# Kernel tuning notes

Hardware: AMD Instinct MI355X
Metric: run time of the kernel (lower is better)

The kernel has to match this reference:

```python
import jax, jax.numpy as jnp
import numpy as np

# CustomConvLayer with a 3x3-tap .kof file, global defaults:
#   operation: x * w, input_encode: x, kernel_encode: w
# => out[b,o,h,w] = sum_c sum_k x_pad[b,c,h+dh_k,w+dw_k] * weights[o,c,k]
# Tap offsets: integer stencil (dh,dw) in {0,1,2}^2 (k_elems=9), padding=1, stride=1.

PAD = 1
TAPS = [(dh, dw) for dh in range(3) for dw in range(3)]  # 9 taps


def setup_inputs() -> dict:
    key = jax.random.key(0)
    k1, k2 = jax.random.split(key)
    x = jax.random.normal(k1, (16, 64, 128, 128), dtype=jnp.float32)
    # learned per-tap weights: [out_channels, in_channels, k_elems]
    weights = jax.random.normal(k2, (128, 64, 9), dtype=jnp.float32) * 0.05
    return {"x": x, "weights": weights}


def reference(x, weights):
    B, C, H, Wd = x.shape
    xp = jnp.pad(x, ((0, 0), (0, 0), (PAD, PAD), (PAD, PAD)))
    # gather per-tap shifted views: [B, C, K, H, W]
    gathered = jnp.stack([xp[:, :, dh:dh + H, dw:dw + Wd] for dh, dw in TAPS], axis=2)
    # per-tap op x*w, then combine over in_channels and taps
    out = jnp.einsum('bckhw,ock->bohw', gathered, weights)
    return out
```

## Files before the change

### kernel.cpp

```cpp
#include <hip/hip_runtime.h>
#include <hip/hip_bf16.h>
#include <stdint.h>


typedef __bf16 bf16x8 __attribute__((ext_vector_type(8)));
typedef float  f32x4  __attribute__((ext_vector_type(4)));

#define GLD_TO_LDS16(g, l)                                                        \
  __builtin_amdgcn_global_load_lds((const __attribute__((address_space(1))) void*)(g), \
                                   (__attribute__((address_space(3))) void*)(l), 16, 0, 0)

__global__ __launch_bounds__(256) void xform_xw(const float* __restrict__ x,
                                                const float* __restrict__ wgt,
                                                __bf16* __restrict__ xpad,
                                                __bf16* __restrict__ BtF) {
  __shared__ float tile[64][129];
  const int tid = threadIdx.x;
  const int b = blockIdx.x >> 7;
  const int h = blockIdx.x & 127;

  {
    const int t = blockIdx.x * 256 + tid;
    if (t < 9216) {
      const int s = t >> 9, rem = t & 511, quad = rem >> 7, n = rem & 127;
      bf16x8 o;
#pragma unroll
      for (int r = 0; r < 8; ++r) {
        const int k = s * 32 + quad * 8 + r;
        const int tap = k >> 6, c = k & 63;
        o[r] = (__bf16)wgt[(n * 64 + c) * 9 + tap];
      }
      *(bf16x8*)(BtF + (size_t)t * 8) = o;
    }
  }

  const bf16x8 z8 = {};
  __bf16* prow = xpad + (size_t)(b * 130 + h + 1) * 8320;
  if (tid < 8)        *(bf16x8*)(prow + tid * 8) = z8;
  else if (tid < 16)  *(bf16x8*)(prow + 8256 + (tid - 8) * 8) = z8;
  if (h == 0) {
    bf16x8* r0 = (bf16x8*)(xpad + (size_t)(b * 130) * 8320);
    for (int i = tid; i < 1040; i += 256) r0[i] = z8;
  } else if (h == 127) {
    bf16x8* r129 = (bf16x8*)(xpad + (size_t)(b * 130 + 129) * 8320);
    for (int i = tid; i < 1040; i += 256) r129[i] = z8;
  }

  const float* src = x + (((size_t)b * 64) * 128 + h) * 128;
  for (int i = tid; i < 2048; i += 256) {
    const int c = i >> 5, w4 = i & 31;
    f32x4 v = *(const f32x4*)(src + (size_t)c * 16384 + w4 * 4);
    tile[c][w4 * 4 + 0] = v[0];
    tile[c][w4 * 4 + 1] = v[1];
    tile[c][w4 * 4 + 2] = v[2];
    tile[c][w4 * 4 + 3] = v[3];
  }
  __syncthreads();
  __bf16* dst = xpad + ((size_t)(b * 130 + h + 1) * 130 + 1) * 64;
  for (int i = tid; i < 1024; i += 256) {
    const int w = i >> 3, cg = i & 7;
    bf16x8 o;
#pragma unroll
    for (int r = 0; r < 8; ++r) o[r] = (__bf16)tile[cg * 8 + r][w];
    *(bf16x8*)(dst + (size_t)w * 64 + cg * 8) = o;
  }
}

__global__ __launch_bounds__(256) void conv_mfma(const __bf16* __restrict__ xpad,
                                                 const __bf16* __restrict__ BtF,
                                                 float* __restrict__ out) {
  __shared__ alignas(16) __bf16 Aslab[3328 * 8];
  const int tid  = threadIdx.x;
  const int lane = tid & 63;
  const int wave = tid >> 6;
  const int quad = lane >> 4;
  const int l16  = lane & 15;
  const int rank = (blockIdx.x & 7) * 256 + (blockIdx.x >> 3);
  const int b = rank >> 7;
  const int h = rank & 127;
  const int wm = wave >> 1;
  const int wn = wave & 1;

  const __bf16* slab = xpad + ((size_t)(b * 130 + h) * 130) * 64;
#define STAGE_UNIT(U) do {                                                \
    const int l_   = ((U) << 8) + tid;                                    \
    const int v_   = l_ >> 3;                                             \
    const int vc_  = v_ > 389 ? 389 : v_;                                 \
    const int cqs_ = (l_ & 7) ^ (v_ & 7);                                 \
    GLD_TO_LDS16(slab + vc_ * 64 + cqs_ * 8,                              \
                 (char*)Aslab + ((((U) << 2) + wave) << 10));             \
  } while (0)

#pragma unroll
  for (int u = 0; u < 13; ++u) STAGE_UNIT(u);
  __builtin_amdgcn_sched_barrier(0);

  f32x4 acc[4][4] = {};

#define PHASE(DH)                                                              \
  _Pragma("unroll")                                                            \
  for (int dw = 0; dw < 3; ++dw) {                                             \
    _Pragma("unroll")                                                          \
    for (int half = 0; half < 2; ++half) {                                     \
      const int s_  = ((DH) * 3 + dw) * 2 + half;                              \
      const int cq_ = (half << 2) + quad;                                      \
      bf16x8 aF[4], bF[4];          \
      _Pragma("unroll")                                                        \
      for (int i = 0; i < 4; ++i) {                                            \
        const int m_    = (wm << 6) + (i << 4) + l16;                          \
        const int v_    = (DH) * 130 + m_ + dw;                                \
        const int slot_ = (v_ << 3) + (cq_ ^ (v_ & 7));                        \
        aF[i] = *(const bf16x8*)(Aslab + (size_t)slot_ * 8);                   \
        const int n_ = (wn << 6) + (i << 4) + l16;                             \
        bF[i] = *(const bf16x8*)(BtF + ((size_t)((s_ * 4 + quad) * 128 + n_) << 3)); \
      }                                                                        \
      _Pragma("unroll")                                                        \
      for (int i = 0; i < 4; ++i)                                              \
        _Pragma("unroll")                                                      \
        for (int j = 0; j < 4; ++j)                                            \
          acc[i][j] = __builtin_amdgcn_mfma_f32_16x16x32_bf16(aF[i], bF[j],    \
                                                              acc[i][j], 0, 0, 0); \
    }                                                                          \
  }

  asm volatile("s_waitcnt vmcnt(8)" ::: "memory");
  __builtin_amdgcn_s_barrier();
  __builtin_amdgcn_sched_barrier(0);
  PHASE(0)
  asm volatile("s_waitcnt vmcnt(4)" ::: "memory");
  __builtin_amdgcn_s_barrier();
  __builtin_amdgcn_sched_barrier(0);
  PHASE(1)
  asm volatile("s_waitcnt vmcnt(0)" ::: "memory");
  __builtin_amdgcn_s_barrier();
  __builtin_amdgcn_sched_barrier(0);
  PHASE(2)

#pragma unroll
  for (int j = 0; j < 4; ++j) {
    const int n = (wn << 6) + (j << 4) + l16;
    float* orow = out + (((size_t)(b * 128 + n) * 128 + h) << 7);
#pragma unroll
    for (int i = 0; i < 4; ++i) {
      const int m0 = (wm << 6) + (i << 4) + (quad << 2);
      *(f32x4*)(orow + m0) = acc[i][j];
    }
  }
}

__global__ void conv_naive(const float* __restrict__ x, const float* __restrict__ wgt,
                           float* __restrict__ out, int total) {
  int idx = blockIdx.x * 256 + threadIdx.x;
  if (idx >= total) return;
  const int w = idx & 127;
  const int h = (idx >> 7) & 127;
  const int o = (idx >> 14) & 127;
  const int b = idx >> 21;
  float s = 0.f;
  for (int c = 0; c < 64; ++c) {
    const float* xc = x + ((size_t)(b * 64 + c) * 128) * 128;
    const float* wc = wgt + (o * 64 + c) * 9;
    for (int dh = 0; dh < 3; ++dh) {
      const int hh = h + dh - 1;
      if (hh < 0 || hh >= 128) continue;
      for (int dw = 0; dw < 3; ++dw) {
        const int ww = w + dw - 1;
        if (ww < 0 || ww >= 128) continue;
        s += xc[hh * 128 + ww] * wc[dh * 3 + dw];
      }
    }
  }
  out[idx] = s;
}

extern "C" void kernel_launch(void* const* d_in, const int* in_sizes, int n_in,
                              void* d_out, int out_size, void* d_ws, size_t ws_size,
                              hipStream_t stream) {
  const float* x   = (const float*)d_in[0];
  const float* wgt = (const float*)d_in[1];
  float* out = (float*)d_out;

  const size_t BTF_BYTES  = 9216ull * 16;
  const size_t XPAD_BYTES = 16ull * 130 * 130 * 64 * sizeof(__bf16);

  if (ws_size < BTF_BYTES + XPAD_BYTES) {
    const int total = 16 * 128 * 128 * 128;
    conv_naive<<<(total + 255) / 256, 256, 0, stream>>>(x, wgt, out, total);
    return;
  }

  __bf16* BtF  = (__bf16*)d_ws;
  __bf16* xpad = (__bf16*)((char*)d_ws + BTF_BYTES);

  xform_xw<<<16 * 128, 256, 0, stream>>>(x, wgt, xpad, BtF);
  conv_mfma<<<16 * 128, 256, 0, stream>>>(xpad, BtF, out);
}
```

Measured before the change: 215.6 us.

## Stage weight fragments into LDS with a triple-buffered per-step pipeline

B (weight) fragments were previously read straight from global memory inside the MFMA loop. They are now streamed into a 3-slot LDS ring using global_load_lds, interleaved with the A slab loads. The compute is split into 18 steps, each with its own vmcnt wait and barrier, and each step prefetches the weight slice two steps ahead. The goal is to take global-load latency off the MFMA critical path. The cost is a larger LDS footprint, which may lower occupancy, plus 18 block barriers per tile.

```diff
diff --git a/kernel.cpp b/kernel.cpp
--- a/kernel.cpp
+++ b/kernel.cpp
@@ -69,7 +69,7 @@
 __global__ __launch_bounds__(256) void conv_mfma(const __bf16* __restrict__ xpad,
                                                  const __bf16* __restrict__ BtF,
                                                  float* __restrict__ out) {
-  __shared__ alignas(16) __bf16 Aslab[3328 * 8];
+  __shared__ alignas(16) __bf16 Aslab[4864 * 8];
   const int tid  = threadIdx.x;
   const int lane = tid & 63;
   const int wave = tid >> 6;
@@ -82,7 +82,8 @@
   const int wn = wave & 1;
 
   const __bf16* slab = xpad + ((size_t)(b * 130 + h) * 130) * 64;
-#define STAGE_UNIT(U) do {                                                \
+
+#define STAGE_A(U) do {                                                   \
     const int l_   = ((U) << 8) + tid;                                    \
     const int v_   = l_ >> 3;                                             \
     const int vc_  = v_ > 389 ? 389 : v_;                                 \
@@ -91,28 +92,41 @@
                  (char*)Aslab + ((((U) << 2) + wave) << 10));             \
   } while (0)
 
-#pragma unroll
-  for (int u = 0; u < 13; ++u) STAGE_UNIT(u);
+#define STAGE_S(K, U) do {                                                \
+    const int c_ = ((U) << 8) + (wave << 6) + lane;                       \
+    GLD_TO_LDS16(BtF + ((size_t)(((K) << 9) + c_) << 3),                  \
+                 (char*)Aslab + ((3328 + (((K) % 3) << 9) + ((U) << 8) + (wave << 6)) << 4)); \
+  } while (0)
+
+  STAGE_A(0); STAGE_A(1); STAGE_A(2); STAGE_A(3); STAGE_A(4);
+  STAGE_S(0, 0); STAGE_S(0, 1);
+  STAGE_S(1, 0); STAGE_S(1, 1);
+  STAGE_A(5); STAGE_A(6); STAGE_A(7); STAGE_A(8);
+  STAGE_S(2, 0); STAGE_S(2, 1);
+  STAGE_A(9); STAGE_A(10); STAGE_A(11); STAGE_A(12);
   __builtin_amdgcn_sched_barrier(0);
 
   f32x4 acc[4][4] = {};
 
-#define PHASE(DH)                                                              \
-  _Pragma("unroll")                                                            \
-  for (int dw = 0; dw < 3; ++dw) {                                             \
-    _Pragma("unroll")                                                          \
-    for (int half = 0; half < 2; ++half) {                                     \
-      const int s_  = ((DH) * 3 + dw) * 2 + half;                              \
-      const int cq_ = (half << 2) + quad;                                      \
+#define STEP(S, VM) do {                                                       \
+    asm volatile("s_waitcnt vmcnt(" #VM ")" ::: "memory");                     \
+    __builtin_amdgcn_s_barrier();                                              \
+    __builtin_amdgcn_sched_barrier(0);                                         \
+    if ((S) >= 1 && (S) <= 15) { STAGE_S((S) + 2, 0); STAGE_S((S) + 2, 1); }   \
+    __builtin_amdgcn_sched_barrier(0);                                         \
+    {                                                                          \
+      const int dh_ = (S) / 6, dw_ = ((S) % 6) >> 1, half_ = (S) & 1;          \
+      const int cq_ = (half_ << 2) + quad;                                     \
       bf16x8 aF[4], bF[4];          \
       _Pragma("unroll")                                                        \
       for (int i = 0; i < 4; ++i) {                                            \
         const int m_    = (wm << 6) + (i << 4) + l16;                          \
-        const int v_    = (DH) * 130 + m_ + dw;                                \
+        const int v_    = dh_ * 130 + m_ + dw_;                                \
         const int slot_ = (v_ << 3) + (cq_ ^ (v_ & 7));                        \
         aF[i] = *(const bf16x8*)(Aslab + (size_t)slot_ * 8);                   \
-        const int n_ = (wn << 6) + (i << 4) + l16;                             \
-        bF[i] = *(const bf16x8*)(BtF + ((size_t)((s_ * 4 + quad) * 128 + n_) << 3)); \
+        bF[i] = *(const bf16x8*)(Aslab +                                       \
+            ((size_t)(3328 + (((S) % 3) << 9) + (quad << 7) + (wn << 6) +      \
+                      (i << 4) + l16) << 3));                                  \
       }                                                                        \
       _Pragma("unroll")                                                        \
       for (int i = 0; i < 4; ++i)                                              \
@@ -121,20 +135,14 @@
           acc[i][j] = __builtin_amdgcn_mfma_f32_16x16x32_bf16(aF[i], bF[j],    \
                                                               acc[i][j], 0, 0, 0); \
     }                                                                          \
-  }
-
-  asm volatile("s_waitcnt vmcnt(8)" ::: "memory");
-  __builtin_amdgcn_s_barrier();
-  __builtin_amdgcn_sched_barrier(0);
-  PHASE(0)
-  asm volatile("s_waitcnt vmcnt(4)" ::: "memory");
-  __builtin_amdgcn_s_barrier();
-  __builtin_amdgcn_sched_barrier(0);
-  PHASE(1)
-  asm volatile("s_waitcnt vmcnt(0)" ::: "memory");
-  __builtin_amdgcn_s_barrier();
-  __builtin_amdgcn_sched_barrier(0);
-  PHASE(2)
+  } while (0)
+
+  STEP(0, 12);  STEP(1, 10);  STEP(2, 6);
+  STEP(3, 2);   STEP(4, 2);   STEP(5, 2);
+  STEP(6, 2);   STEP(7, 2);   STEP(8, 2);
+  STEP(9, 2);   STEP(10, 2);  STEP(11, 2);
+  STEP(12, 2);  STEP(13, 2);  STEP(14, 2);
+  STEP(15, 2);  STEP(16, 2);  STEP(17, 0);
 
 #pragma unroll
   for (int j = 0; j < 4; ++j) {
```

Measured after the change: 214.6 us. No clear change (-0.5%).
